# Optimization experiments

Measured on AMD Instinct MI355X. Metric: run time of the kernel, lower is better.

The kernel has to match this reference:

```python
import jax, jax.numpy as jnp
import numpy as np

EPS = 1e-6
SCAL = 5.0
PARTS = 16
NFEAT = 32
RES = 64


def conv(x, w, b, stride=1):
    y = jax.lax.conv_general_dilated(x, w, (stride, stride), 'SAME',
                                     dimension_numbers=('NCHW', 'OIHW', 'NCHW'))
    return y + b[None, :, None, None]


def spatial_softmax(x):
    b, k, h, w = x.shape
    return jax.nn.softmax(x.reshape(b, k, h * w), axis=-1).reshape(b, k, h, w)


def make_grid(h, w):
    ys = jnp.linspace(-1.0, 1.0, h)
    xs = jnp.linspace(-1.0, 1.0, w)
    gy, gx = jnp.meshgrid(ys, xs, indexing='ij')
    return jnp.stack([gy, gx], axis=-1)  # [h, w, 2]


def e_sigma(x, w1, b1, w2, b2, wp, bp):
    # shared shape/appearance encoder: parts via spatial softmax + residual sum map
    h1 = jax.nn.relu(conv(x, w1, b1, stride=2))   # [B,64,64,64]
    h2 = jax.nn.relu(conv(h1, w2, b2))            # [B,64,64,64]
    parts = spatial_softmax(conv(h2, wp, bp))     # [B,16,64,64]
    return parts, h2


def e_alpha(x, w1, b1, w2, b2):
    h1 = jax.nn.relu(conv(x, w1, b1))
    return conv(h1, w2, b2)                       # [B,32,64,64]


def get_mu_and_prec(parts):
    # soft-argmax mean + 2x2 covariance -> inverse Cholesky factor L_inv
    b, k, h, w = parts.shape
    grid = make_grid(h, w)
    mu = jnp.einsum('bkhw,hwc->bkc', parts, grid)                       # [b,k,2]
    outer = jnp.einsum('hwm,hwn->hwmn', grid, grid)
    cov = jnp.einsum('bkhw,hwmn->bkmn', parts, outer) - jnp.einsum('bkm,bkn->bkmn', mu, mu)
    a = jnp.sqrt(cov[..., 0, 0] + EPS)
    bb = cov[..., 0, 1] / (a + EPS)
    c = jnp.sqrt(jnp.maximum(cov[..., 1, 1] - bb * bb, 0.0) + EPS)
    det = a * c
    z = jnp.zeros_like(a)
    L_inv = SCAL / (det[..., None, None] + EPS) * jnp.stack(
        [jnp.stack([c, z], axis=-1), jnp.stack([-bb, a], axis=-1)], axis=-2)  # [b,k,2,2]
    return mu, L_inv


def feat_mu_to_enc(alpha, mu, L_inv, h, w):
    # render Cauchy-shaped part heatmaps from (mu, L_inv) and paint part features
    grid = make_grid(h, w)
    dist = grid[None, None] - mu[:, :, None, None, :]        # [b,k,h,w,2]
    proj = jnp.einsum('bkhwi,bkij->bkhwj', dist, L_inv)
    heat = 1.0 / (1.0 + jnp.sum(proj * proj, axis=-1))       # [b,k,h,w]
    norm = heat / (jnp.sum(heat, axis=(2, 3), keepdims=True) + EPS)
    fmap = jnp.einsum('bkf,bkhw->bfhw', alpha, norm)         # [b,nf,h,w]
    return jnp.concatenate([heat, fmap], axis=1)             # [b,nk+nf,h,w]


def decoder(enc, w1, b1, w2, b2, w3, b3):
    h1 = jax.nn.relu(conv(enc, w1, b1))                      # [B,64,64,64]
    up = jnp.repeat(jnp.repeat(h1, 2, axis=2), 2, axis=3)    # nearest upsample -> 128
    h2 = jax.nn.relu(conv(up, w2, b2))
    return jax.nn.sigmoid(conv(h2, w3, b3))                  # [B,3,128,128]


def setup_inputs():
    key = jax.random.key(0)
    ks = jax.random.split(key, 16)
    def w(k, shape):
        fan_in = shape[1] * shape[2] * shape[3]
        return (jax.random.normal(k, shape, jnp.float32) / np.sqrt(fan_in)).astype(jnp.float32)
    B = 32
    return {
        'x': jax.random.uniform(ks[0], (B, 3, 128, 128), jnp.float32),
        'x_spatial_transform': jax.random.uniform(ks[1], (B, 3, 128, 128), jnp.float32),
        'x_appearance_transform': jax.random.uniform(ks[2], (B, 3, 128, 128), jnp.float32),
        'coord': jax.random.normal(ks[3], (B, PARTS, 2), jnp.float32) * 0.5,
        'vector': jax.random.normal(ks[4], (B, PARTS, 2), jnp.float32) * 0.1,
        'es_w1': w(ks[5], (RES, 3, 3, 3)), 'es_b1': jnp.zeros((RES,), jnp.float32),
        'es_w2': w(ks[6], (RES, RES, 3, 3)), 'es_b2': jnp.zeros((RES,), jnp.float32),
        'es_wp': w(ks[7], (PARTS, RES, 3, 3)), 'es_bp': jnp.zeros((PARTS,), jnp.float32),
        'ea_w1': w(ks[8], (RES, RES, 3, 3)), 'ea_b1': jnp.zeros((RES,), jnp.float32),
        'ea_w2': w(ks[9], (NFEAT, RES, 3, 3)), 'ea_b2': jnp.zeros((NFEAT,), jnp.float32),
        'd_w1': w(ks[10], (RES, PARTS + NFEAT, 3, 3)), 'd_b1': jnp.zeros((RES,), jnp.float32),
        'd_w2': w(ks[11], (32, RES, 3, 3)), 'd_b2': jnp.zeros((32,), jnp.float32),
        'd_w3': w(ks[12], (3, 32, 3, 3)), 'd_b3': jnp.zeros((3,), jnp.float32),
    }


def reference(x, x_spatial_transform, x_appearance_transform, coord, vector,
              es_w1, es_b1, es_w2, es_b2, es_wp, es_bp,
              ea_w1, ea_b1, ea_w2, ea_b2,
              d_w1, d_b1, d_w2, d_b2, d_w3, d_b3):
    # shape stream (appearance-transformed image -> geometry)
    shape_parts, _ = e_sigma(x_appearance_transform, es_w1, es_b1, es_w2, es_b2, es_wp, es_bp)
    mu, L_inv = get_mu_and_prec(shape_parts)
    # appearance stream (spatially-transformed image -> appearance)
    app_parts, app_sum = e_sigma(x_spatial_transform, es_w1, es_b1, es_w2, es_b2, es_wp, es_bp)
    f_xs = e_alpha(app_sum, ea_w1, ea_b1, ea_w2, ea_b2)
    # local part appearances: gather features under each part map
    alpha = jnp.einsum('bfhw,bkhw->bkf', f_xs, app_parts)
    encoding = feat_mu_to_enc(alpha, mu, L_inv, 64, 64)
    reconstruction = decoder(encoding, d_w1, d_b1, d_w2, d_b2, d_w3, d_b3)
    # composite loss
    mu_a, L_inv_a = get_mu_and_prec(app_parts)
    rec_loss = jnp.mean((x - reconstruction) ** 2)
    equiv_loss = jnp.mean((mu - mu_a) ** 2) + 0.01 * jnp.mean((L_inv - L_inv_a) ** 2)
    transport_loss = jnp.mean((mu_a - (coord + vector)) ** 2)
    loss = rec_loss + equiv_loss + transport_loss
    return reconstruction, loss
```

## Files before the change

### kernel.cpp

```cpp
#include <hip/hip_runtime.h>
#include <hip/hip_bf16.h>

#define EPS 1e-6f
#define SCAL 5.0f

typedef __attribute__((ext_vector_type(8))) short bf8v;
typedef __attribute__((ext_vector_type(4))) float f32x4;

#define OFF_MU     0
#define OFF_LINV   1024
#define OFF_MUA    3072
#define OFF_LINVA  4096
#define OFF_HSUM   6144
#define OFF_ALPHA  6656
#define OFF_REC    23040
#define OFF_R1     32768
#define OFF_R2     (OFF_R1 + 8388608)
#define OFF_R3     (OFF_R2 + 8388608)
#define WS_TOTAL   (OFF_R3 + 16777216)

#define BA_XA   ((size_t)2 * OFF_R3)
#define BA_X2   ((size_t)2 * OFF_R1)
#define OFF_PARTSF OFF_R2
#define OFF_PROBS  (OFF_R2 + 4194304)
#define BA_EA1  ((size_t)2 * OFF_R3)
#define OFF_FXS (OFF_R3 + 4194304)
#define BA_E    ((size_t)2 * OFF_R2)
#define BA_D1   ((size_t)2 * OFF_R1)
#define BA_D2   ((size_t)2 * OFF_R3)

#define WT_ESW1 0
#define WT_ESB1 1728
#define WT_ESB2 1792
#define WT_ESBP 1856
#define WT_EAB1 1872
#define WT_EAB2 1936
#define WT_DB1  1968
#define WT_DB2  2032
#define WT_W3P  2064
#define WT_DB3  2928
#define P_WP2  0
#define P_WPP  36864
#define P_WPA1 46080
#define P_WPA2 82944
#define P_WPD1 101376
#define P_WPD2 138240

__device__ __attribute__((aligned(16))) float g_ws[WS_TOTAL];
__device__ __attribute__((aligned(16))) float g_wt[3072];
__device__ __attribute__((aligned(16))) __hip_bfloat16 g_wp[156672];
__device__ int g_isbf16;

__device__ __forceinline__ float selz(bool c, float v) { return c ? v : 0.f; }
__device__ __forceinline__ float cvtbf(short s) {
    return __uint_as_float(((unsigned int)(unsigned short)s) << 16);
}
__device__ __forceinline__ float ldin(const void* p, size_t i, int bf) {
    return bf ? __bfloat162float(((const __hip_bfloat16*)p)[i])
              : ((const float*)p)[i];
}

__device__ __forceinline__ float block_sum(float v) {
    __shared__ float sb[8];
    for (int off = 32; off; off >>= 1) v += __shfl_down(v, off, 64);
    int lane = threadIdx.x & 63, wid = threadIdx.x >> 6;
    __syncthreads();
    if (lane == 0) sb[wid] = v;
    __syncthreads();
    float r = 0.f;
    for (int i = 0; i < 4; ++i) r += sb[i];
    return r;
}
__device__ __forceinline__ float block_max(float v) {
    __shared__ float sb[8];
    for (int off = 32; off; off >>= 1) v = fmaxf(v, __shfl_down(v, off, 64));
    int lane = threadIdx.x & 63, wid = threadIdx.x >> 6;
    __syncthreads();
    if (lane == 0) sb[wid] = v;
    __syncthreads();
    float r = -1e30f;
    for (int i = 0; i < 4; ++i) r = fmaxf(r, sb[i]);
    return r;
}

__global__ void detect_k(const void* x) {
    const __hip_bfloat16* p = (const __hip_bfloat16*)x;
    int lane = threadIdx.x & 63;
    float v = 0.f;
    for (int i = lane; i < 256; i += 64) {
        float a = fabsf(__bfloat162float(p[i]));
        if (!(a <= 2.0f)) v = 1.f;
    }
    for (int off = 32; off; off >>= 1) v += __shfl_down(v, off, 64);
    if (lane == 0) {
        g_isbf16 = (v == 0.f) ? 1 : 0;
        g_ws[OFF_REC] = 0.f;
    }
}

__global__ void wpack_k(const void* esw1, const void* esb1, const void* esw2, const void* esb2,
                        const void* eswp, const void* esbp, const void* eaw1, const void* eab1,
                        const void* eaw2, const void* eab2, const void* dw1, const void* db1,
                        const void* dw2, const void* db2, const void* dw3, const void* db3) {
    int bf = g_isbf16;
    int gid0 = blockIdx.x * 256 + threadIdx.x, stride = gridDim.x * 256;
    for (int g = gid0; g < 1728; g += stride) g_wt[WT_ESW1 + g] = ldin(esw1, g, bf);
    for (int g = gid0; g < 64; g += stride) g_wt[WT_ESB1 + g] = ldin(esb1, g, bf);
    for (int g = gid0; g < 64; g += stride) g_wt[WT_ESB2 + g] = ldin(esb2, g, bf);
    for (int g = gid0; g < 16; g += stride) g_wt[WT_ESBP + g] = ldin(esbp, g, bf);
    for (int g = gid0; g < 64; g += stride) g_wt[WT_EAB1 + g] = ldin(eab1, g, bf);
    for (int g = gid0; g < 32; g += stride) g_wt[WT_EAB2 + g] = ldin(eab2, g, bf);
    for (int g = gid0; g < 64; g += stride) g_wt[WT_DB1 + g] = ldin(db1, g, bf);
    for (int g = gid0; g < 32; g += stride) g_wt[WT_DB2 + g] = ldin(db2, g, bf);
    for (int g = gid0; g < 3; g += stride) g_wt[WT_DB3 + g] = ldin(db3, g, bf);
    for (int g = gid0; g < 864; g += stride) {
        int t = g / 96, o = (g / 32) % 3, k = g & 31;
        g_wt[WT_W3P + g] = ldin(dw3, (size_t)(o * 32 + k) * 9 + t, bf);
    }
    for (int g = gid0; g < 36864; g += stride) {
        int t = g >> 12, n = (g >> 6) & 63, k = g & 63;
        g_wp[P_WP2 + g] = __float2bfloat16(ldin(esw2, (size_t)(n * 64 + k) * 9 + t, bf));
    }
    for (int g = gid0; g < 9216; g += stride) {
        int t = g >> 10, n = (g >> 6) & 15, k = g & 63;
        g_wp[P_WPP + g] = __float2bfloat16(ldin(eswp, (size_t)(n * 64 + k) * 9 + t, bf));
    }
    for (int g = gid0; g < 36864; g += stride) {
        int t = g >> 12, n = (g >> 6) & 63, k = g & 63;
        g_wp[P_WPA1 + g] = __float2bfloat16(ldin(eaw1, (size_t)(n * 64 + k) * 9 + t, bf));
    }
    for (int g = gid0; g < 18432; g += stride) {
        int t = g >> 11, n = (g >> 6) & 31, k = g & 63;
        g_wp[P_WPA2 + g] = __float2bfloat16(ldin(eaw2, (size_t)(n * 64 + k) * 9 + t, bf));
    }
    for (int g = gid0; g < 36864; g += stride) {
        int t = g >> 12, n = (g >> 6) & 63, k = g & 63;
        float v = (k < 48) ? ldin(dw1, (size_t)(n * 48 + k) * 9 + t, bf) : 0.f;
        g_wp[P_WPD1 + g] = __float2bfloat16(v);
    }
    for (int g = gid0; g < 18432; g += stride) {
        int t = g >> 11, n = (g >> 6) & 31, k = g & 63;
        g_wp[P_WPD2 + g] = __float2bfloat16(ldin(dw2, (size_t)(n * 64 + k) * 9 + t, bf));
    }
}

__global__ void __launch_bounds__(256)
conv_s2n_k(const void* __restrict__ inA, const void* __restrict__ inB) {
    int bf = g_isbf16;
    int tile = blockIdx.x & 15;
    int gb = blockIdx.x >> 4;
    int g = gb & 3, b = gb >> 2;
    const void* in = (b < 32) ? inA : inB;
    int bb = b & 31;
    int pix = tile * 256 + threadIdx.x;
    int y = pix >> 6, x = pix & 63;
    size_t inb = (size_t)bb * 3 * 16384;
    const float* W = g_wt + WT_ESW1 + (size_t)(g * 16) * 27;
    float acc[16];
    #pragma unroll
    for (int o = 0; o < 16; ++o) acc[o] = g_wt[WT_ESB1 + g * 16 + o];
    int iy0 = 2 * y, ix0 = 2 * x;
    bool my2 = (iy0 + 2 < 128), mx2 = (ix0 + 2 < 128);
    int iy2 = my2 ? iy0 + 2 : 127, ix2 = mx2 ? ix0 + 2 : 127;
    for (int ic = 0; ic < 3; ++ic) {
        size_t pb = inb + ic * 16384;
        float t[9];
        t[0] = ldin(in, pb + iy0 * 128 + ix0, bf);
        t[1] = ldin(in, pb + iy0 * 128 + ix0 + 1, bf);
        t[2] = selz(mx2, ldin(in, pb + iy0 * 128 + ix2, bf));
        t[3] = ldin(in, pb + (iy0 + 1) * 128 + ix0, bf);
        t[4] = ldin(in, pb + (iy0 + 1) * 128 + ix0 + 1, bf);
        t[5] = selz(mx2, ldin(in, pb + (iy0 + 1) * 128 + ix2, bf));
        t[6] = selz(my2, ldin(in, pb + iy2 * 128 + ix0, bf));
        t[7] = selz(my2, ldin(in, pb + iy2 * 128 + ix0 + 1, bf));
        t[8] = selz(my2 && mx2, ldin(in, pb + iy2 * 128 + ix2, bf));
        #pragma unroll
        for (int o = 0; o < 16; ++o) {
            const float* wr = W + (o * 3 + ic) * 9;
            float a = acc[o];
            #pragma unroll
            for (int j = 0; j < 9; ++j) a = fmaf(t[j], wr[j], a);
            acc[o] = a;
        }
    }
    __hip_bfloat16* out = (__hip_bfloat16*)g_ws + BA_XA + ((size_t)b * 4096 + pix) * 64 + g * 16;
    #pragma unroll
    for (int o = 0; o < 16; ++o) out[o] = __float2bfloat16(fmaxf(acc[o], 0.f));
}

__device__ __forceinline__ void stage_tile(__hip_bfloat16* sA,
                                           const __hip_bfloat16* __restrict__ inb, int y0) {
    for (int g = threadIdx.x; g < 3072; g += 256) {
        int r = g >> 9;
        int rem = g & 511;
        int px = rem >> 3, j = rem & 7;
        int yy = y0 - 1 + r;
        int P = px + 1;
        bf8v v = (bf8v){0, 0, 0, 0, 0, 0, 0, 0};
        if (yy >= 0 && yy <= 63)
            v = *(const bf8v*)(inb + ((size_t)(yy * 64 + px) * 64 + j * 8));
        *(bf8v*)(sA + ((r * 66 + P) * 64 + ((j ^ (P & 7)) * 8))) = v;
    }
    if (threadIdx.x < 96) {
        int g = threadIdx.x;
        int r = g / 16, rem = g % 16, side = rem >> 3, j = rem & 7;
        int P = side ? 65 : 0;
        *(bf8v*)(sA + ((r * 66 + P) * 64 + ((j ^ (P & 7)) * 8))) = (bf8v){0, 0, 0, 0, 0, 0, 0, 0};
    }
}

template<int TOTN, int NS, int OUTF32, int RELU>
__device__ __forceinline__ void conv_body(const __hip_bfloat16* sA, int bO, int y,
                                          int wid, int l15, int quad,
                                          int wp_off, int bias_off, size_t out_off) {
    f32x4 acc[4][NS];
    #pragma unroll
    for (int ms = 0; ms < 4; ++ms)
        #pragma unroll
        for (int ns = 0; ns < NS; ++ns) acc[ms][ns] = (f32x4){0.f, 0.f, 0.f, 0.f};

    if constexpr (NS == 1) {
        bf8v bw[18];
        #pragma unroll
        for (int it = 0; it < 18; ++it) {
            const int t = it >> 1, c = it & 1;
            bw[it] = *(const bf8v*)(g_wp + wp_off +
                     ((size_t)(t * TOTN + l15) * 64 + c * 32 + quad * 8));
        }
        #pragma unroll
        for (int it = 0; it < 18; ++it) {
            const int t = it >> 1, c = it & 1;
            const int dy = t / 3 - 1, dx = t % 3 - 1;
            const int r = wid + 1 + dy;
            const int j = c * 4 + quad;
            #pragma unroll
            for (int ms = 0; ms < 4; ++ms) {
                int P = ms * 16 + l15 + dx + 1;
                bf8v a = *(const bf8v*)(sA + ((r * 66 + P) * 64 + ((j ^ (P & 7)) * 8)));
                acc[ms][0] = __builtin_amdgcn_mfma_f32_16x16x32_bf16(a, bw[it], acc[ms][0], 0, 0, 0);
            }
        }
    } else {
        bf8v bq[2][NS];
        #pragma unroll
        for (int ns = 0; ns < NS; ++ns)
            bq[0][ns] = *(const bf8v*)(g_wp + wp_off +
                        ((size_t)(ns * 16 + l15) * 64 + quad * 8));
        #pragma unroll
        for (int it = 0; it < 18; ++it) {
            const int t = it >> 1, c = it & 1;
            if (it + 1 < 18) {
                const int t2 = (it + 1) >> 1, c2 = (it + 1) & 1;
                #pragma unroll
                for (int ns = 0; ns < NS; ++ns)
                    bq[(it + 1) & 1][ns] = *(const bf8v*)(g_wp + wp_off +
                        ((size_t)(t2 * TOTN + ns * 16 + l15) * 64 + c2 * 32 + quad * 8));
            }
            const int dy = t / 3 - 1, dx = t % 3 - 1;
            const int r = wid + 1 + dy;
            const int j = c * 4 + quad;
            bf8v a[4];
            #pragma unroll
            for (int ms = 0; ms < 4; ++ms) {
                int P = ms * 16 + l15 + dx + 1;
                a[ms] = *(const bf8v*)(sA + ((r * 66 + P) * 64 + ((j ^ (P & 7)) * 8)));
            }
            #pragma unroll
            for (int ns = 0; ns < NS; ++ns)
                #pragma unroll
                for (int ms = 0; ms < 4; ++ms)
                    acc[ms][ns] = __builtin_amdgcn_mfma_f32_16x16x32_bf16(a[ms], bq[it & 1][ns], acc[ms][ns], 0, 0, 0);
        }
    }

    #pragma unroll
    for (int ns = 0; ns < NS; ++ns) {
        float bias = g_wt[bias_off + ns * 16 + l15];
        #pragma unroll
        for (int ms = 0; ms < 4; ++ms) {
            #pragma unroll
            for (int r = 0; r < 4; ++r) {
                int pix = ms * 16 + quad * 4 + r;
                float v = acc[ms][ns][r] + bias;
                if (RELU) v = fmaxf(v, 0.f);
                size_t o = out_off + ((size_t)(bO * 4096 + y * 64 + pix)) * TOTN + ns * 16 + l15;
                if (OUTF32) g_ws[o] = v;
                else ((__hip_bfloat16*)g_ws)[o] = __float2bfloat16(v);
            }
        }
    }
}

template<int TOTN, int NS, int OUTF32, int RELU>
__global__ void __launch_bounds__(256) __attribute__((amdgpu_waves_per_eu(2, 4)))
conv_mfl_k(size_t in_off, int wp_off, int bias_off, size_t out_off) {
    __shared__ __hip_bfloat16 sA[6 * 66 * 64];
    int wid = threadIdx.x >> 6, lane = threadIdx.x & 63;
    int l15 = lane & 15, quad = lane >> 4;
    int b = blockIdx.x >> 4, y0 = (blockIdx.x & 15) * 4;
    const __hip_bfloat16* inb = (const __hip_bfloat16*)g_ws + in_off + (size_t)b * 4096 * 64;
    stage_tile(sA, inb, y0);
    __syncthreads();
    conv_body<TOTN, NS, OUTF32, RELU>(sA, b, y0 + wid, wid, l15, quad,
                                      wp_off, bias_off, out_off);
}

__global__ void __launch_bounds__(256) __attribute__((amdgpu_waves_per_eu(2, 4)))
conv_pea_k() {
    __shared__ __hip_bfloat16 sA[6 * 66 * 64];
    int wid = threadIdx.x >> 6, lane = threadIdx.x & 63;
    int l15 = lane & 15, quad = lane >> 4;
    int b = blockIdx.x >> 4, y0 = (blockIdx.x & 15) * 4;
    const __hip_bfloat16* inb = (const __hip_bfloat16*)g_ws + BA_X2 + (size_t)b * 4096 * 64;
    stage_tile(sA, inb, y0);
    __syncthreads();
    int y = y0 + wid;
    conv_body<16, 1, 1, 0>(sA, b, y, wid, l15, quad, P_WPP, WT_ESBP, (size_t)OFF_PARTSF);
    if (b >= 32)
        conv_body<64, 4, 0, 1>(sA, b - 32, y, wid, l15, quad, P_WPA1, WT_EAB1, BA_EA1);
}

__global__ void __launch_bounds__(256) __attribute__((amdgpu_waves_per_eu(2, 4)))
conv_upmf2_k(size_t in_off, int wp_off, int bias_off, size_t out_off) {
    __shared__ __hip_bfloat16 sA[4 * 66 * 64];
    int wid = threadIdx.x >> 6, lane = threadIdx.x & 63;
    int l15 = lane & 15, quad = lane >> 4;
    int b = blockIdx.x >> 5, y0 = (blockIdx.x & 31) * 4;
    int ri0 = (y0 >> 1) - 1;
    const __hip_bfloat16* inb = (const __hip_bfloat16*)g_ws + in_off + (size_t)b * 4096 * 64;
    for (int g = threadIdx.x; g < 2048; g += 256) {
        int r = g >> 9;
        int rem = g & 511;
        int px = rem >> 3, j = rem & 7;
        int yi = ri0 + r;
        int P = px + 1;
        bf8v v = (bf8v){0, 0, 0, 0, 0, 0, 0, 0};
        if (yi >= 0 && yi <= 63)
            v = *(const bf8v*)(inb + ((size_t)(yi * 64 + px) * 64 + j * 8));
        *(bf8v*)(sA + ((r * 66 + P) * 64 + ((j ^ (P & 7)) * 8))) = v;
    }
    if (threadIdx.x < 64) {
        int g = threadIdx.x;
        int r = g >> 4, rem = g & 15, side = rem >> 3, j = rem & 7;
        int P = side ? 65 : 0;
        *(bf8v*)(sA + ((r * 66 + P) * 64 + ((j ^ (P & 7)) * 8))) = (bf8v){0, 0, 0, 0, 0, 0, 0, 0};
    }
    __syncthreads();
    int y = y0 + wid;
    f32x4 acc[8][2];
    #pragma unroll
    for (int ms = 0; ms < 8; ++ms)
        #pragma unroll
        for (int ns = 0; ns < 2; ++ns) acc[ms][ns] = (f32x4){0.f, 0.f, 0.f, 0.f};
    bf8v bq[2][2];
    #pragma unroll
    for (int ns = 0; ns < 2; ++ns)
        bq[0][ns] = *(const bf8v*)(g_wp + wp_off + ((size_t)(ns * 16 + l15) * 64 + quad * 8));
    #pragma unroll
    for (int it = 0; it < 18; ++it) {
        const int t = it >> 1, c = it & 1;
        if (it + 1 < 18) {
            const int t2 = (it + 1) >> 1, c2 = (it + 1) & 1;
            #pragma unroll
            for (int ns = 0; ns < 2; ++ns)
                bq[(it + 1) & 1][ns] = *(const bf8v*)(g_wp + wp_off +
                    ((size_t)(t2 * 32 + ns * 16 + l15) * 64 + c2 * 32 + quad * 8));
        }
        const int dy = t / 3 - 1, dx = t % 3 - 1;
        int yy = y + dy;
        if (yy >= 0 && yy <= 127) {
            int r = (yy >> 1) - ri0;
            int j = c * 4 + quad;
            bf8v a[8];
            #pragma unroll
            for (int ms = 0; ms < 8; ++ms) {
                int xx = ms * 16 + l15 + dx;
                int P = (xx < 0) ? 0 : ((xx > 127) ? 65 : ((xx >> 1) + 1));
                a[ms] = *(const bf8v*)(sA + ((r * 66 + P) * 64 + ((j ^ (P & 7)) * 8)));
            }
            #pragma unroll
            for (int ns = 0; ns < 2; ++ns)
                #pragma unroll
                for (int ms = 0; ms < 8; ++ms)
                    acc[ms][ns] = __builtin_amdgcn_mfma_f32_16x16x32_bf16(a[ms], bq[it & 1][ns], acc[ms][ns], 0, 0, 0);
        }
    }
    #pragma unroll
    for (int ns = 0; ns < 2; ++ns) {
        float bias = g_wt[bias_off + ns * 16 + l15];
        #pragma unroll
        for (int ms = 0; ms < 8; ++ms) {
            #pragma unroll
            for (int r = 0; r < 4; ++r) {
                int pix = ms * 16 + quad * 4 + r;
                float v = fmaxf(acc[ms][ns][r] + bias, 0.f);
                size_t o = out_off + ((size_t)(b * 16384 + y * 128 + pix)) * 32 + ns * 16 + l15;
                ((__hip_bfloat16*)g_ws)[o] = __float2bfloat16(v);
            }
        }
    }
}

__global__ void sm_mom3_k() {
    int bk = blockIdx.x;
    int b = bk >> 4, k = bk & 15;
    int app = (b >= 32);
    const float* P = g_ws + OFF_PARTSF + (size_t)b * 4096 * 16 + k;
    float r[16];
    #pragma unroll
    for (int j = 0; j < 16; ++j) r[j] = P[(size_t)(threadIdx.x + j * 256) * 16];
    float m = r[0];
    #pragma unroll
    for (int j = 1; j < 16; ++j) m = fmaxf(m, r[j]);
    m = block_max(m);
    float s = 0.f;
    #pragma unroll
    for (int j = 0; j < 16; ++j) { r[j] = __expf(r[j] - m); s += r[j]; }
    s = block_sum(s);
    float inv = 1.0f / s;
    float sy = 0, sx = 0, syy = 0, sxy = 0, sxx = 0;
    #pragma unroll
    for (int j = 0; j < 16; ++j) {
        float pv = r[j] * inv;
        int i = threadIdx.x + j * 256;
        if (app) g_ws[OFF_PROBS + ((size_t)(b - 32) * 16 + k) * 4096 + i] = pv;
        float gy = -1.0f + (i >> 6) * (2.0f / 63.0f);
        float gx = -1.0f + (i & 63) * (2.0f / 63.0f);
        sy += pv * gy; sx += pv * gx;
        syy += pv * gy * gy; sxy += pv * gy * gx; sxx += pv * gx * gx;
    }
    sy = block_sum(sy); sx = block_sum(sx);
    syy = block_sum(syy); sxy = block_sum(sxy); sxx = block_sum(sxx);
    if (threadIdx.x == 0) {
        float c00 = syy - sy * sy, c01 = sxy - sy * sx, c11 = sxx - sx * sx;
        float a = sqrtf(fmaxf(c00 + EPS, 1e-12f));
        float bb = c01 / (a + EPS);
        float cc = sqrtf(fmaxf(c11 - bb * bb, 0.f) + EPS);
        float det = a * cc;
        float sc = SCAL / (det + EPS);
        int idx = app ? ((b - 32) * 16 + k) : (b * 16 + k);
        int mu_off = app ? OFF_MUA : OFF_MU;
        int linv_off = app ? OFF_LINVA : OFF_LINV;
        g_ws[mu_off + idx * 2 + 0] = sy;
        g_ws[mu_off + idx * 2 + 1] = sx;
        g_ws[linv_off + idx * 4 + 0] = cc * sc;
        g_ws[linv_off + idx * 4 + 1] = 0.f;
        g_ws[linv_off + idx * 4 + 2] = -bb * sc;
        g_ws[linv_off + idx * 4 + 3] = a * sc;
    }
}

__global__ void alpha2_k() {
    int bk = blockIdx.x;
    int b = bk >> 4;
    __shared__ float pl[4096];
    const float* pr = g_ws + OFF_PROBS + (size_t)bk * 4096;
    for (int i = threadIdx.x; i < 4096; i += 256) pl[i] = pr[i];
    __syncthreads();
    float acc[32];
    #pragma unroll
    for (int f = 0; f < 32; ++f) acc[f] = 0.f;
    for (int i = threadIdx.x; i < 4096; i += 256) {
        float pv = pl[i];
        const float* fp = g_ws + OFF_FXS + (size_t)(b * 4096 + i) * 32;
        #pragma unroll
        for (int f = 0; f < 32; ++f) acc[f] = fmaf(pv, fp[f], acc[f]);
    }
    __shared__ float sw[4][32];
    int lane = threadIdx.x & 63, wid = threadIdx.x >> 6;
    #pragma unroll
    for (int f = 0; f < 32; ++f)
        for (int off = 32; off; off >>= 1) acc[f] += __shfl_down(acc[f], off, 64);
    if (lane == 0) {
        #pragma unroll
        for (int f = 0; f < 32; ++f) sw[wid][f] = acc[f];
    }
    __syncthreads();
    if (threadIdx.x < 32)
        g_ws[OFF_ALPHA + bk * 32 + threadIdx.x] =
            sw[0][threadIdx.x] + sw[1][threadIdx.x] + sw[2][threadIdx.x] + sw[3][threadIdx.x];
}

__global__ void heat2_k() {
    int bk = blockIdx.x;
    int b = bk >> 4, k = bk & 15;
    float m0 = g_ws[OFF_MU + bk * 2], m1 = g_ws[OFF_MU + bk * 2 + 1];
    float L00 = g_ws[OFF_LINV + bk * 4 + 0], L10 = g_ws[OFF_LINV + bk * 4 + 2],
          L11 = g_ws[OFF_LINV + bk * 4 + 3];
    __hip_bfloat16* E = (__hip_bfloat16*)g_ws + BA_E;
    float s = 0.f;
    for (int i = threadIdx.x; i < 4096; i += 256) {
        float d0 = -1.0f + (i >> 6) * (2.0f / 63.0f) - m0;
        float d1 = -1.0f + (i & 63) * (2.0f / 63.0f) - m1;
        float p0 = d0 * L00 + d1 * L10;
        float p1 = d1 * L11;
        float h = 1.0f / (1.0f + p0 * p0 + p1 * p1);
        E[(size_t)(b * 4096 + i) * 64 + k] = __float2bfloat16(h);
        s += h;
    }
    s = block_sum(s);
    if (threadIdx.x == 0) g_ws[OFF_HSUM + bk] = s;
}

__global__ void fmap2_k() {
    int tile = blockIdx.x & 15, b = blockIdx.x >> 4;
    __shared__ float coef[16][32];
    for (int i = threadIdx.x; i < 512; i += 256) {
        int k = i >> 5, f = i & 31;
        coef[k][f] = g_ws[OFF_ALPHA + (b * 16 + k) * 32 + f] /
                     (g_ws[OFF_HSUM + b * 16 + k] + EPS);
    }
    __syncthreads();
    int pix = tile * 256 + threadIdx.x;
    __hip_bfloat16* E = (__hip_bfloat16*)g_ws + BA_E + (size_t)(b * 4096 + pix) * 64;
    float h[16];
    #pragma unroll
    for (int k = 0; k < 16; ++k) h[k] = __bfloat162float(E[k]);
    #pragma unroll
    for (int f = 0; f < 32; ++f) {
        float a = 0.f;
        #pragma unroll
        for (int k = 0; k < 16; ++k) a = fmaf(h[k], coef[k][f], a);
        E[16 + f] = __float2bfloat16(a);
    }
    #pragma unroll
    for (int z = 48; z < 64; ++z) E[z] = __float2bfloat16(0.f);
}

__global__ void __launch_bounds__(256)
conv_sign_k(const void* __restrict__ ximg, void* __restrict__ outp) {
    int bf = g_isbf16;
    int tile = blockIdx.x & 63, b = blockIdx.x >> 6;
    int pix = tile * 256 + threadIdx.x;
    int y = pix >> 7, x = pix & 127;
    const short* D2 = (const short*)((const __hip_bfloat16*)g_ws + BA_D2 + (size_t)b * 16384 * 32);
    float acc[3];
    #pragma unroll
    for (int o = 0; o < 3; ++o) acc[o] = g_wt[WT_DB3 + o];
    #pragma unroll
    for (int t = 0; t < 9; ++t) {
        int dy = t / 3 - 1, dx = t % 3 - 1;
        int yy = y + dy, xx = x + dx;
        if (yy < 0 || yy > 127 || xx < 0 || xx > 127) continue;
        const short* sp = D2 + (size_t)(yy * 128 + xx) * 32;
        #pragma unroll
        for (int c = 0; c < 4; ++c) {
            bf8v v = *(const bf8v*)(sp + c * 8);
            #pragma unroll
            for (int j = 0; j < 8; ++j) {
                float av = cvtbf(v[j]);
                int k = c * 8 + j;
                acc[0] = fmaf(av, g_wt[WT_W3P + (t * 3 + 0) * 32 + k], acc[0]);
                acc[1] = fmaf(av, g_wt[WT_W3P + (t * 3 + 1) * 32 + k], acc[1]);
                acc[2] = fmaf(av, g_wt[WT_W3P + (t * 3 + 2) * 32 + k], acc[2]);
            }
        }
    }
    float es = 0.f;
    #pragma unroll
    for (int o = 0; o < 3; ++o) {
        float v = 1.0f / (1.0f + __expf(-acc[o]));
        size_t oidx = ((size_t)b * 3 + o) * 16384 + pix;
        if (bf) ((__hip_bfloat16*)outp)[oidx] = __float2bfloat16(v);
        else    ((float*)outp)[oidx] = v;
        float e = ldin(ximg, oidx, bf) - v;
        es += e * e;
    }
    float s = block_sum(es);
    if (threadIdx.x == 0) atomicAdd(&g_ws[OFF_REC], s);
}

__global__ void loss_k(const void* __restrict__ coord,
                       const void* __restrict__ vec,
                       void* __restrict__ outp) {
    int bf = g_isbf16;
    const float* mu = g_ws + OFF_MU;
    const float* linv = g_ws + OFF_LINV;
    const float* mu_a = g_ws + OFF_MUA;
    const float* linv_a = g_ws + OFF_LINVA;
    float s1 = 0, s2 = 0, s3 = 0;
    for (int i = threadIdx.x; i < 1024; i += 256) {
        float d = mu[i] - mu_a[i];
        s1 += d * d;
        float t = ldin(coord, i, bf) + ldin(vec, i, bf);
        float d3 = mu_a[i] - t;
        s3 += d3 * d3;
    }
    for (int i = threadIdx.x; i < 2048; i += 256) {
        float d = linv[i] - linv_a[i];
        s2 += d * d;
    }
    s1 = block_sum(s1);
    s2 = block_sum(s2);
    s3 = block_sum(s3);
    if (threadIdx.x == 0) {
        float loss = g_ws[OFF_REC] / 1572864.0f + s1 / 1024.0f + 0.01f * (s2 / 2048.0f)
                   + s3 / 1024.0f;
        if (bf) ((__hip_bfloat16*)outp)[1572864] = __float2bfloat16(loss);
        else    ((float*)outp)[1572864] = loss;
    }
}

extern "C" void kernel_launch(void* const* d_in, const int* in_sizes, int n_in,
                              void* d_out, int out_size, void* d_ws, size_t ws_size,
                              hipStream_t stream) {
    const void* x     = d_in[0];
    const void* x_st  = d_in[1];
    const void* x_at  = d_in[2];
    const void* coord = d_in[3];
    const void* vec   = d_in[4];

    dim3 blk(256);

    detect_k<<<1, 64, 0, stream>>>(x);
    wpack_k<<<64, blk, 0, stream>>>(
        d_in[5],  d_in[6],  d_in[7],  d_in[8],
        d_in[9],  d_in[10], d_in[11], d_in[12],
        d_in[13], d_in[14], d_in[15], d_in[16],
        d_in[17], d_in[18], d_in[19], d_in[20]);

    conv_s2n_k<<<64 * 4 * 16, blk, 0, stream>>>(x_at, x_st);
    conv_mfl_k<64, 4, 0, 1><<<1024, blk, 0, stream>>>(BA_XA, P_WP2, WT_ESB2, BA_X2);

    conv_pea_k<<<1024, blk, 0, stream>>>();
    sm_mom3_k<<<1024, blk, 0, stream>>>();

    conv_mfl_k<32, 2, 1, 0><<<512, blk, 0, stream>>>(BA_EA1, P_WPA2, WT_EAB2, (size_t)OFF_FXS);
    alpha2_k<<<512, blk, 0, stream>>>();

    heat2_k<<<512, blk, 0, stream>>>();
    fmap2_k<<<512, blk, 0, stream>>>();

    conv_mfl_k<64, 4, 0, 1><<<512, blk, 0, stream>>>(BA_E, P_WPD1, WT_DB1, BA_D1);
    conv_upmf2_k<<<1024, blk, 0, stream>>>(BA_D1, P_WPD2, WT_DB2, BA_D2);
    conv_sign_k<<<32 * 64, blk, 0, stream>>>(x, d_out);

    loss_k<<<1, blk, 0, stream>>>(coord, vec, d_out);
}
```

Measured before the change: 452.2 us.

## Halve conv LDS tiles by staging channel halves, raise occupancy, rework heat kernel

The 3x3 MFMA convolutions now stage their input in two 32-channel halves, which halves shared memory per block. Launch bounds now target four blocks per unit, and the 32-image convs use 2-row tiles to double the block count. Block-to-image mapping is swapped so neighbouring blocks work on different images. The parts map output is stored channel-major so the softmax kernel reads contiguous data. heat2 now processes a pixel tile across all 16 parts with vector bf16 stores and atomic sums, replacing the per-part strided scalar stores; this adds an extra barrier per conv and relies on atomics with the sum buffer zeroed in wpack.

```diff
diff --git a/kernel.cpp b/kernel.cpp
--- a/kernel.cpp
+++ b/kernel.cpp
@@ -55,6 +55,11 @@
 __device__ __forceinline__ float cvtbf(short s) {
     return __uint_as_float(((unsigned int)(unsigned short)s) << 16);
 }
+__device__ __forceinline__ short f2bf(float f) {
+    unsigned u = __float_as_uint(f);
+    u += 0x7fff + ((u >> 16) & 1);
+    return (short)(u >> 16);
+}
 __device__ __forceinline__ float ldin(const void* p, size_t i, int bf) {
     return bf ? __bfloat162float(((const __hip_bfloat16*)p)[i])
               : ((const float*)p)[i];
@@ -104,6 +109,7 @@
                         const void* dw2, const void* db2, const void* dw3, const void* db3) {
     int bf = g_isbf16;
     int gid0 = blockIdx.x * 256 + threadIdx.x, stride = gridDim.x * 256;
+    for (int g = gid0; g < 512; g += stride) g_ws[OFF_HSUM + g] = 0.f;
     for (int g = gid0; g < 1728; g += stride) g_wt[WT_ESW1 + g] = ldin(esw1, g, bf);
     for (int g = gid0; g < 64; g += stride) g_wt[WT_ESB1 + g] = ldin(esb1, g, bf);
     for (int g = gid0; g < 64; g += stride) g_wt[WT_ESB2 + g] = ldin(esb2, g, bf);
@@ -188,99 +194,91 @@
     for (int o = 0; o < 16; ++o) out[o] = __float2bfloat16(fmaxf(acc[o], 0.f));
 }
 
-__device__ __forceinline__ void stage_tile(__hip_bfloat16* sA,
-                                           const __hip_bfloat16* __restrict__ inb, int y0) {
-    for (int g = threadIdx.x; g < 3072; g += 256) {
-        int r = g >> 9;
-        int rem = g & 511;
-        int px = rem >> 3, j = rem & 7;
+template<int TR>
+__device__ __forceinline__ void stage_half(__hip_bfloat16* sA,
+                                           const __hip_bfloat16* __restrict__ inb,
+                                           int y0, int c) {
+    constexpr int CH = TR * 256;
+    for (int g = threadIdx.x; g < CH; g += 256) {
+        int r = g >> 8;
+        int rem = g & 255;
+        int px = rem >> 2, j = rem & 3;
         int yy = y0 - 1 + r;
         int P = px + 1;
         bf8v v = (bf8v){0, 0, 0, 0, 0, 0, 0, 0};
         if (yy >= 0 && yy <= 63)
-            v = *(const bf8v*)(inb + ((size_t)(yy * 64 + px) * 64 + j * 8));
-        *(bf8v*)(sA + ((r * 66 + P) * 64 + ((j ^ (P & 7)) * 8))) = v;
-    }
-    if (threadIdx.x < 96) {
+            v = *(const bf8v*)(inb + ((size_t)(yy * 64 + px) * 64 + c * 32 + j * 8));
+        *(bf8v*)(sA + ((r * 66 + P) * 32 + ((j ^ (P & 3)) * 8))) = v;
+    }
+    if (threadIdx.x < TR * 8) {
         int g = threadIdx.x;
-        int r = g / 16, rem = g % 16, side = rem >> 3, j = rem & 7;
+        int r = g >> 3, rem = g & 7, side = rem >> 2, j = rem & 3;
         int P = side ? 65 : 0;
-        *(bf8v*)(sA + ((r * 66 + P) * 64 + ((j ^ (P & 7)) * 8))) = (bf8v){0, 0, 0, 0, 0, 0, 0, 0};
-    }
-}
-
-template<int TOTN, int NS, int OUTF32, int RELU>
-__device__ __forceinline__ void conv_body(const __hip_bfloat16* sA, int bO, int y,
-                                          int wid, int l15, int quad,
-                                          int wp_off, int bias_off, size_t out_off) {
-    f32x4 acc[4][NS];
-    #pragma unroll
-    for (int ms = 0; ms < 4; ++ms)
-        #pragma unroll
-        for (int ns = 0; ns < NS; ++ns) acc[ms][ns] = (f32x4){0.f, 0.f, 0.f, 0.f};
-
-    if constexpr (NS == 1) {
-        bf8v bw[18];
-        #pragma unroll
-        for (int it = 0; it < 18; ++it) {
-            const int t = it >> 1, c = it & 1;
-            bw[it] = *(const bf8v*)(g_wp + wp_off +
-                     ((size_t)(t * TOTN + l15) * 64 + c * 32 + quad * 8));
-        }
-        #pragma unroll
-        for (int it = 0; it < 18; ++it) {
-            const int t = it >> 1, c = it & 1;
-            const int dy = t / 3 - 1, dx = t % 3 - 1;
-            const int r = wid + 1 + dy;
-            const int j = c * 4 + quad;
-            #pragma unroll
-            for (int ms = 0; ms < 4; ++ms) {
-                int P = ms * 16 + l15 + dx + 1;
-                bf8v a = *(const bf8v*)(sA + ((r * 66 + P) * 64 + ((j ^ (P & 7)) * 8)));
-                acc[ms][0] = __builtin_amdgcn_mfma_f32_16x16x32_bf16(a, bw[it], acc[ms][0], 0, 0, 0);
-            }
-        }
-    } else {
+        *(bf8v*)(sA + ((r * 66 + P) * 32 + ((j ^ (P & 3)) * 8))) = (bf8v){0, 0, 0, 0, 0, 0, 0, 0};
+    }
+}
+
+template<int TOTN, int NS, int MS, int PF>
+__device__ __forceinline__ void body9(const __hip_bfloat16* sA, int c, int rowIn, int pxb,
+                                      int l15, int quad, int wp_off, f32x4 (&acc)[MS][NS]) {
+    if constexpr (PF) {
         bf8v bq[2][NS];
         #pragma unroll
         for (int ns = 0; ns < NS; ++ns)
             bq[0][ns] = *(const bf8v*)(g_wp + wp_off +
-                        ((size_t)(ns * 16 + l15) * 64 + quad * 8));
-        #pragma unroll
-        for (int it = 0; it < 18; ++it) {
-            const int t = it >> 1, c = it & 1;
-            if (it + 1 < 18) {
-                const int t2 = (it + 1) >> 1, c2 = (it + 1) & 1;
+                        ((size_t)(ns * 16 + l15) * 64 + c * 32 + quad * 8));
+        #pragma unroll
+        for (int t = 0; t < 9; ++t) {
+            if (t < 8) {
                 #pragma unroll
                 for (int ns = 0; ns < NS; ++ns)
-                    bq[(it + 1) & 1][ns] = *(const bf8v*)(g_wp + wp_off +
-                        ((size_t)(t2 * TOTN + ns * 16 + l15) * 64 + c2 * 32 + quad * 8));
+                    bq[(t + 1) & 1][ns] = *(const bf8v*)(g_wp + wp_off +
+                        ((size_t)((t + 1) * TOTN + ns * 16 + l15) * 64 + c * 32 + quad * 8));
             }
             const int dy = t / 3 - 1, dx = t % 3 - 1;
-            const int r = wid + 1 + dy;
-            const int j = c * 4 + quad;
-            bf8v a[4];
-            #pragma unroll
-            for (int ms = 0; ms < 4; ++ms) {
-                int P = ms * 16 + l15 + dx + 1;
-                a[ms] = *(const bf8v*)(sA + ((r * 66 + P) * 64 + ((j ^ (P & 7)) * 8)));
+            const int r = rowIn + 1 + dy;
+            #pragma unroll
+            for (int ms = 0; ms < MS; ++ms) {
+                int P = pxb + ms * 16 + l15 + dx + 1;
+                bf8v a = *(const bf8v*)(sA + ((r * 66 + P) * 32 + ((quad ^ (P & 3)) * 8)));
+                #pragma unroll
+                for (int ns = 0; ns < NS; ++ns)
+                    acc[ms][ns] = __builtin_amdgcn_mfma_f32_16x16x32_bf16(a, bq[t & 1][ns], acc[ms][ns], 0, 0, 0);
             }
+        }
+    } else {
+        #pragma unroll
+        for (int t = 0; t < 9; ++t) {
+            bf8v bv[NS];
             #pragma unroll
             for (int ns = 0; ns < NS; ++ns)
+                bv[ns] = *(const bf8v*)(g_wp + wp_off +
+                         ((size_t)(t * TOTN + ns * 16 + l15) * 64 + c * 32 + quad * 8));
+            const int dy = t / 3 - 1, dx = t % 3 - 1;
+            const int r = rowIn + 1 + dy;
+            #pragma unroll
+            for (int ms = 0; ms < MS; ++ms) {
+                int P = pxb + ms * 16 + l15 + dx + 1;
+                bf8v a = *(const bf8v*)(sA + ((r * 66 + P) * 32 + ((quad ^ (P & 3)) * 8)));
                 #pragma unroll
-                for (int ms = 0; ms < 4; ++ms)
-                    acc[ms][ns] = __builtin_amdgcn_mfma_f32_16x16x32_bf16(a[ms], bq[it & 1][ns], acc[ms][ns], 0, 0, 0);
-        }
-    }
-
+                for (int ns = 0; ns < NS; ++ns)
+                    acc[ms][ns] = __builtin_amdgcn_mfma_f32_16x16x32_bf16(a, bv[ns], acc[ms][ns], 0, 0, 0);
+            }
+        }
+    }
+}
+
+template<int TOTN, int NS, int MS, int OUTF32, int RELU>
+__device__ __forceinline__ void epi_std(f32x4 (&acc)[MS][NS], int bO, int y, int pxb,
+                                        int l15, int quad, int bias_off, size_t out_off) {
     #pragma unroll
     for (int ns = 0; ns < NS; ++ns) {
         float bias = g_wt[bias_off + ns * 16 + l15];
         #pragma unroll
-        for (int ms = 0; ms < 4; ++ms) {
+        for (int ms = 0; ms < MS; ++ms) {
             #pragma unroll
             for (int r = 0; r < 4; ++r) {
-                int pix = ms * 16 + quad * 4 + r;
+                int pix = pxb + ms * 16 + quad * 4 + r;
                 float v = acc[ms][ns][r] + bias;
                 if (RELU) v = fmaxf(v, 0.f);
                 size_t o = out_off + ((size_t)(bO * 4096 + y * 64 + pix)) * TOTN + ns * 16 + l15;
@@ -291,33 +289,72 @@
     }
 }
 
-template<int TOTN, int NS, int OUTF32, int RELU>
-__global__ void __launch_bounds__(256) __attribute__((amdgpu_waves_per_eu(2, 4)))
-conv_mfl_k(size_t in_off, int wp_off, int bias_off, size_t out_off) {
-    __shared__ __hip_bfloat16 sA[6 * 66 * 64];
+template<int TOTN, int NS, int OUTF32, int RELU, int HALF>
+__global__ void __launch_bounds__(256, 4)
+conv_mfl2_k(size_t in_off, int wp_off, int bias_off, size_t out_off) {
+    constexpr int ROWS = HALF ? 2 : 4;
+    constexpr int TR = ROWS + 2;
+    constexpr int MS = HALF ? 2 : 4;
+    __shared__ __hip_bfloat16 sA[TR * 66 * 32];
     int wid = threadIdx.x >> 6, lane = threadIdx.x & 63;
     int l15 = lane & 15, quad = lane >> 4;
-    int b = blockIdx.x >> 4, y0 = (blockIdx.x & 15) * 4;
+    int b = HALF ? (blockIdx.x & 31) : (blockIdx.x & 63);
+    int y0 = (int)(blockIdx.x >> (HALF ? 5 : 6)) * ROWS;
+    int rowIn = HALF ? (wid >> 1) : wid;
+    int pxb = HALF ? ((wid & 1) * 32) : 0;
+    int y = y0 + rowIn;
     const __hip_bfloat16* inb = (const __hip_bfloat16*)g_ws + in_off + (size_t)b * 4096 * 64;
-    stage_tile(sA, inb, y0);
-    __syncthreads();
-    conv_body<TOTN, NS, OUTF32, RELU>(sA, b, y0 + wid, wid, l15, quad,
-                                      wp_off, bias_off, out_off);
-}
-
-__global__ void __launch_bounds__(256) __attribute__((amdgpu_waves_per_eu(2, 4)))
-conv_pea_k() {
-    __shared__ __hip_bfloat16 sA[6 * 66 * 64];
+    f32x4 acc[MS][NS];
+    #pragma unroll
+    for (int ms = 0; ms < MS; ++ms)
+        #pragma unroll
+        for (int ns = 0; ns < NS; ++ns) acc[ms][ns] = (f32x4){0.f, 0.f, 0.f, 0.f};
+    #pragma unroll
+    for (int c = 0; c < 2; ++c) {
+        if (c) __syncthreads();
+        stage_half<TR>(sA, inb, y0, c);
+        __syncthreads();
+        body9<TOTN, NS, MS, 1>(sA, c, rowIn, pxb, l15, quad, wp_off, acc);
+    }
+    epi_std<TOTN, NS, MS, OUTF32, RELU>(acc, b, y, pxb, l15, quad, bias_off, out_off);
+}
+
+__global__ void __launch_bounds__(256, 4)
+conv_pea2_k() {
+    __shared__ __hip_bfloat16 sA[6 * 66 * 32];
     int wid = threadIdx.x >> 6, lane = threadIdx.x & 63;
     int l15 = lane & 15, quad = lane >> 4;
-    int b = blockIdx.x >> 4, y0 = (blockIdx.x & 15) * 4;
+    int b = blockIdx.x & 63;
+    int y0 = (int)(blockIdx.x >> 6) * 4;
+    int y = y0 + wid;
+    int app = (b >= 32);
     const __hip_bfloat16* inb = (const __hip_bfloat16*)g_ws + BA_X2 + (size_t)b * 4096 * 64;
-    stage_tile(sA, inb, y0);
-    __syncthreads();
-    int y = y0 + wid;
-    conv_body<16, 1, 1, 0>(sA, b, y, wid, l15, quad, P_WPP, WT_ESBP, (size_t)OFF_PARTSF);
-    if (b >= 32)
-        conv_body<64, 4, 0, 1>(sA, b - 32, y, wid, l15, quad, P_WPA1, WT_EAB1, BA_EA1);
+    f32x4 accP[4][1];
+    f32x4 accE[4][4];
+    #pragma unroll
+    for (int ms = 0; ms < 4; ++ms) {
+        accP[ms][0] = (f32x4){0.f, 0.f, 0.f, 0.f};
+        #pragma unroll
+        for (int ns = 0; ns < 4; ++ns) accE[ms][ns] = (f32x4){0.f, 0.f, 0.f, 0.f};
+    }
+    #pragma unroll
+    for (int c = 0; c < 2; ++c) {
+        if (c) __syncthreads();
+        stage_half<6>(sA, inb, y0, c);
+        __syncthreads();
+        body9<16, 1, 4, 1>(sA, c, wid, 0, l15, quad, P_WPP, accP);
+        if (app) body9<64, 4, 4, 0>(sA, c, wid, 0, l15, quad, P_WPA1, accE);
+    }
+    float biasP = g_wt[WT_ESBP + l15];
+    #pragma unroll
+    for (int ms = 0; ms < 4; ++ms)
+        #pragma unroll
+        for (int r = 0; r < 4; ++r) {
+            int pix = ms * 16 + quad * 4 + r;
+            g_ws[OFF_PARTSF + ((size_t)b * 16 + l15) * 4096 + y * 64 + pix] =
+                accP[ms][0][r] + biasP;
+        }
+    if (app) epi_std<64, 4, 4, 0, 1>(accE, b - 32, y, 0, l15, quad, WT_EAB1, BA_EA1);
 }
 
 __global__ void __launch_bounds__(256) __attribute__((amdgpu_waves_per_eu(2, 4)))
@@ -403,12 +440,12 @@
 
 __global__ void sm_mom3_k() {
     int bk = blockIdx.x;
-    int b = bk >> 4, k = bk & 15;
+    int b = bk >> 4;
     int app = (b >= 32);
-    const float* P = g_ws + OFF_PARTSF + (size_t)b * 4096 * 16 + k;
+    const float* P = g_ws + OFF_PARTSF + (size_t)bk * 4096;
     float r[16];
     #pragma unroll
-    for (int j = 0; j < 16; ++j) r[j] = P[(size_t)(threadIdx.x + j * 256) * 16];
+    for (int j = 0; j < 16; ++j) r[j] = P[threadIdx.x * 16 + j];
     float m = r[0];
     #pragma unroll
     for (int j = 1; j < 16; ++j) m = fmaxf(m, r[j]);
@@ -422,8 +459,8 @@
     #pragma unroll
     for (int j = 0; j < 16; ++j) {
         float pv = r[j] * inv;
-        int i = threadIdx.x + j * 256;
-        if (app) g_ws[OFF_PROBS + ((size_t)(b - 32) * 16 + k) * 4096 + i] = pv;
+        int i = threadIdx.x * 16 + j;
+        if (app) g_ws[OFF_PROBS + (size_t)(bk - 512) * 4096 + i] = pv;
         float gy = -1.0f + (i >> 6) * (2.0f / 63.0f);
         float gx = -1.0f + (i & 63) * (2.0f / 63.0f);
         sy += pv * gy; sx += pv * gx;
@@ -438,7 +475,7 @@
         float cc = sqrtf(fmaxf(c11 - bb * bb, 0.f) + EPS);
         float det = a * cc;
         float sc = SCAL / (det + EPS);
-        int idx = app ? ((b - 32) * 16 + k) : (b * 16 + k);
+        int idx = app ? (bk - 512) : bk;
         int mu_off = app ? OFF_MUA : OFF_MU;
         int linv_off = app ? OFF_LINVA : OFF_LINV;
         g_ws[mu_off + idx * 2 + 0] = sy;
@@ -451,8 +488,8 @@
 }
 
 __global__ void alpha2_k() {
-    int bk = blockIdx.x;
-    int b = bk >> 4;
+    int b = blockIdx.x & 31, k = blockIdx.x >> 5;
+    int bk = b * 16 + k;
     __shared__ float pl[4096];
     const float* pr = g_ws + OFF_PROBS + (size_t)bk * 4096;
     for (int i = threadIdx.x; i < 4096; i += 256) pl[i] = pr[i];
@@ -482,24 +519,41 @@
 }
 
 __global__ void heat2_k() {
-    int bk = blockIdx.x;
-    int b = bk >> 4, k = bk & 15;
-    float m0 = g_ws[OFF_MU + bk * 2], m1 = g_ws[OFF_MU + bk * 2 + 1];
-    float L00 = g_ws[OFF_LINV + bk * 4 + 0], L10 = g_ws[OFF_LINV + bk * 4 + 2],
-          L11 = g_ws[OFF_LINV + bk * 4 + 3];
-    __hip_bfloat16* E = (__hip_bfloat16*)g_ws + BA_E;
-    float s = 0.f;
-    for (int i = threadIdx.x; i < 4096; i += 256) {
-        float d0 = -1.0f + (i >> 6) * (2.0f / 63.0f) - m0;
-        float d1 = -1.0f + (i & 63) * (2.0f / 63.0f) - m1;
+    int tile = blockIdx.x & 15, b = blockIdx.x >> 4;
+    __shared__ float hs[16];
+    if (threadIdx.x < 16) hs[threadIdx.x] = 0.f;
+    __syncthreads();
+    int pix = tile * 256 + threadIdx.x;
+    float gy = -1.0f + (pix >> 6) * (2.0f / 63.0f);
+    float gx = -1.0f + (pix & 63) * (2.0f / 63.0f);
+    bf8v e0, e1;
+    float hv[16];
+    #pragma unroll
+    for (int k = 0; k < 16; ++k) {
+        int bk = b * 16 + k;
+        float m0 = g_ws[OFF_MU + bk * 2], m1 = g_ws[OFF_MU + bk * 2 + 1];
+        float L00 = g_ws[OFF_LINV + bk * 4 + 0], L10 = g_ws[OFF_LINV + bk * 4 + 2],
+              L11 = g_ws[OFF_LINV + bk * 4 + 3];
+        float d0 = gy - m0, d1 = gx - m1;
         float p0 = d0 * L00 + d1 * L10;
         float p1 = d1 * L11;
         float h = 1.0f / (1.0f + p0 * p0 + p1 * p1);
-        E[(size_t)(b * 4096 + i) * 64 + k] = __float2bfloat16(h);
-        s += h;
-    }
-    s = block_sum(s);
-    if (threadIdx.x == 0) g_ws[OFF_HSUM + bk] = s;
+        hv[k] = h;
+        short sbits = f2bf(h);
+        if (k < 8) e0[k] = sbits; else e1[k - 8] = sbits;
+    }
+    __hip_bfloat16* E = (__hip_bfloat16*)g_ws + BA_E + (size_t)(b * 4096 + pix) * 64;
+    *(bf8v*)E = e0;
+    *(bf8v*)(E + 8) = e1;
+    #pragma unroll
+    for (int k = 0; k < 16; ++k) {
+        float v = hv[k];
+        for (int off = 32; off; off >>= 1) v += __shfl_down(v, off, 64);
+        if ((threadIdx.x & 63) == 0) atomicAdd(&hs[k], v);
+    }
+    __syncthreads();
+    if (threadIdx.x < 16)
+        atomicAdd(&g_ws[OFF_HSUM + b * 16 + threadIdx.x], hs[threadIdx.x]);
 }
 
 __global__ void fmap2_k() {
@@ -620,18 +674,18 @@
         d_in[17], d_in[18], d_in[19], d_in[20]);
 
     conv_s2n_k<<<64 * 4 * 16, blk, 0, stream>>>(x_at, x_st);
-    conv_mfl_k<64, 4, 0, 1><<<1024, blk, 0, stream>>>(BA_XA, P_WP2, WT_ESB2, BA_X2);
-
-    conv_pea_k<<<1024, blk, 0, stream>>>();
+    conv_mfl2_k<64, 4, 0, 1, 0><<<1024, blk, 0, stream>>>(BA_XA, P_WP2, WT_ESB2, BA_X2);
+
+    conv_pea2_k<<<1024, blk, 0, stream>>>();
     sm_mom3_k<<<1024, blk, 0, stream>>>();
 
-    conv_mfl_k<32, 2, 1, 0><<<512, blk, 0, stream>>>(BA_EA1, P_WPA2, WT_EAB2, (size_t)OFF_FXS);
+    conv_mfl2_k<32, 2, 1, 0, 1><<<1024, blk, 0, stream>>>(BA_EA1, P_WPA2, WT_EAB2, (size_t)OFF_FXS);
     alpha2_k<<<512, blk, 0, stream>>>();
 
     heat2_k<<<512, blk, 0, stream>>>();
     fmap2_k<<<512, blk, 0, stream>>>();
 
-    conv_mfl_k<64, 4, 0, 1><<<512, blk, 0, stream>>>(BA_E, P_WPD1, WT_DB1, BA_D1);
+    conv_mfl2_k<64, 4, 0, 1, 1><<<1024, blk, 0, stream>>>(BA_E, P_WPD1, WT_DB1, BA_D1);
     conv_upmf2_k<<<1024, blk, 0, stream>>>(BA_D1, P_WPD2, WT_DB2, BA_D2);
     conv_sign_k<<<32 * 64, blk, 0, stream>>>(x, d_out);
 
```

Result: slower. 593.0 us (+31.1%).
